# Performance work log

Measured on AMD Instinct MI355X. Metric: run time of the kernel, lower is better.

## Reference

```python
import jax, jax.numpy as jnp
import numpy as np

EPS = 1e-6
T_MAX = 0.999  # occlusion threshold used by compute_paths


def _dot(a, b):
    return jnp.sum(a * b, axis=-1)


def _mirror(p, v, n):
    # Reflect point p across plane through v with unit normal n.
    return p - 2.0 * _dot(p - v, n)[..., None] * n


def image_method(frm, to, mirror_v, mirror_n):
    """frm/to: [...,3]; mirror_v/mirror_n: [...,order,3] -> paths [...,order,3]."""
    order = mirror_v.shape[-2]
    images = []
    cur = frm
    for i in range(order):  # forward pass: successive images of TX
        cur = _mirror(cur, mirror_v[..., i, :], mirror_n[..., i, :])
        images.append(cur)
    paths = [None] * order
    nxt = to
    for i in range(order - 1, -1, -1):  # backward pass: intersect with planes
        img = images[i]
        v = mirror_v[..., i, :]
        n = mirror_n[..., i, :]
        d = nxt - img
        denom = _dot(d, n)
        t = _dot(v - img, n) / jnp.where(jnp.abs(denom) < EPS, EPS, denom)
        nxt = img + t[..., None] * d
        paths[i] = nxt
    return jnp.stack(paths, axis=-2)


def triangles_contain(tv, p):
    """tv: [...,3,3] triangle vertices, p: [...,3] point in same plane -> bool."""
    v0, v1, v2 = tv[..., 0, :], tv[..., 1, :], tv[..., 2, :]
    n0 = jnp.cross(p - v0, v1 - v0)
    n1 = jnp.cross(p - v1, v2 - v1)
    n2 = jnp.cross(p - v2, v0 - v2)
    d01, d12, d20 = _dot(n0, n1), _dot(n1, n2), _dot(n2, n0)
    pos = (d01 >= 0) & (d12 >= 0) & (d20 >= 0)
    neg = (d01 <= 0) & (d12 <= 0) & (d20 <= 0)
    return pos | neg


def same_side_of_mirrors(full_paths, mirror_v, mirror_n):
    """full_paths: [...,order+2,3]; consecutive vertices around each mirror on same side."""
    order = mirror_v.shape[-2]
    prev_v = full_paths[..., :order, :]
    next_v = full_paths[..., 2:, :]
    d_prev = _dot(prev_v - mirror_v, mirror_n)
    d_next = _dot(next_v - mirror_v, mirror_n)
    return d_prev * d_next >= 0


def rays_intersect_triangles(o, d, tv):
    """Moller-Trumbore. o,d: [...,3]; tv: broadcastable [...,3,3] -> (t, hit)."""
    v0, v1, v2 = tv[..., 0, :], tv[..., 1, :], tv[..., 2, :]
    e1 = v1 - v0
    e2 = v2 - v0
    h = jnp.cross(d, e2)
    a = _dot(e1, h)
    inv = 1.0 / jnp.where(jnp.abs(a) < EPS, 1.0, a)
    s = o - v0
    u = _dot(s, h) * inv
    q = jnp.cross(s, e1)
    v = _dot(d, q) * inv
    t = _dot(e2, q) * inv
    hit = (jnp.abs(a) > EPS) & (u >= 0.0) & (v >= 0.0) & (u + v <= 1.0) & (t > EPS)
    return t, hit


def compute_paths(transmitters, receivers, vertices, normals, triangles, path_candidates):
    P = path_candidates.shape[0]
    ntx = transmitters.shape[0]
    nrx = receivers.shape[0]
    all_tv = vertices[triangles]  # [T,3,3]

    frm = jnp.broadcast_to(transmitters[None, :, None, :], (P, ntx, nrx, 3))
    to = jnp.broadcast_to(receivers[None, None, :, :], (P, ntx, nrx, 3))

    pc_tv = all_tv[path_candidates]          # [P,order,3,3]
    mirror_v = pc_tv[..., 0, :]              # [P,order,3]
    mirror_n = normals[path_candidates]      # [P,order,3]
    tvb = pc_tv[:, None, None]               # [P,1,1,order,3,3]
    mvb = mirror_v[:, None, None]            # [P,1,1,order,3]
    mnb = mirror_n[:, None, None]

    paths = image_method(frm, to, mvb, mnb)  # [P,ntx,nrx,order,3]
    mask = jnp.all(triangles_contain(tvb, paths), axis=-1)

    full_paths = jnp.concatenate(
        (frm[..., None, :], paths, to[..., None, :]), axis=-2
    )  # [P,ntx,nrx,order+2,3]
    mask = mask & jnp.all(same_side_of_mirrors(full_paths, mvb, mnb), axis=-1)

    # Occlusion test: each of the order+1 segments vs every mesh triangle.
    ray_o = full_paths[..., :-1, None, :]       # [P,ntx,nrx,order+1,1,3]
    ray_d = jnp.diff(full_paths, axis=-2)[..., None, :]
    t, hit = rays_intersect_triangles(ray_o, ray_d, all_tv)  # [P,ntx,nrx,order+1,T]
    intersect = jnp.any((t < T_MAX) & hit, axis=(-1, -2))
    mask = mask & ~intersect

    # jit-friendly masking (original uses boolean fancy-indexing): zero-out invalid paths.
    return jnp.where(mask[..., None, None], full_paths, 0.0)


def setup_inputs() -> dict:
    key = jax.random.key(0)
    k1, k2, k3, k4 = jax.random.split(key, 4)
    V, T = 100, 128
    transmitters = 5.0 * jax.random.normal(k1, (1, 3), jnp.float32)
    receivers = 5.0 * jax.random.normal(k2, (1, 3), jnp.float32)
    vertices = jax.random.uniform(k3, (V, 3), jnp.float32, -10.0, 10.0)
    triangles = jax.random.randint(k4, (T, 3), 0, V, jnp.int32)
    tv = vertices[triangles]
    n = jnp.cross(tv[:, 1] - tv[:, 0], tv[:, 2] - tv[:, 0])
    normals = n / (jnp.linalg.norm(n, axis=-1, keepdims=True) + 1e-8)
    # generate_all_path_candidates(T, order=2): all ordered pairs (i,j), i != j
    idx = np.arange(T)
    ii, jj = np.meshgrid(idx, idx, indexing="ij")
    m = ii != jj
    path_candidates = jnp.asarray(np.stack([ii[m], jj[m]], axis=-1), jnp.int32)
    return {
        "transmitters": transmitters,
        "receivers": receivers,
        "vertices": vertices,
        "normals": normals,
        "triangles": triangles,
        "path_candidates": path_candidates,
        "order": 2,
    }


def reference(transmitters, receivers, vertices, normals, triangles, path_candidates, order):
    del order  # encoded in path_candidates.shape[-1]
    return compute_paths(transmitters, receivers, vertices, normals, triangles, path_candidates)
```

## Files before the change

kernel.cpp:

```cpp
#include <hip/hip_runtime.h>
#include <hip/hip_bf16.h>

#define EPS_F  1e-6f
#define TMAX_F 0.999f

struct F3 { float x, y, z; };

__device__ __forceinline__ F3 operator-(F3 a, F3 b){ return {a.x-b.x, a.y-b.y, a.z-b.z}; }
__device__ __forceinline__ F3 operator+(F3 a, F3 b){ return {a.x+b.x, a.y+b.y, a.z+b.z}; }
__device__ __forceinline__ F3 operator*(float s, F3 a){ return {s*a.x, s*a.y, s*a.z}; }
__device__ __forceinline__ float dot3(F3 a, F3 b){ return a.x*b.x + a.y*b.y + a.z*b.z; }
__device__ __forceinline__ F3 cross3(F3 a, F3 b){
  return { a.y*b.z - a.z*b.y, a.z*b.x - a.x*b.z, a.x*b.y - a.y*b.x };
}
__device__ __forceinline__ F3 ld3(const float* p){ return {p[0], p[1], p[2]}; }

__device__ __forceinline__ F3 mirror3(F3 p, F3 v, F3 n){
  float d = dot3(p - v, n);
  return p - (2.0f * d) * n;
}

__device__ __forceinline__ F3 plane_pt(F3 img, F3 v, F3 n, F3 nxt){
  F3 d = nxt - img;
  float den = dot3(d, n);
  float sd = (fabsf(den) < EPS_F) ? EPS_F : den;
  float t = dot3(v - img, n) / sd;
  return img + t * d;
}

__device__ __forceinline__ bool tri_contains(const float* tv9, F3 p){
  F3 a = ld3(tv9), b = ld3(tv9+3), c = ld3(tv9+6);
  F3 n0 = cross3(p - a, b - a);
  F3 n1 = cross3(p - b, c - b);
  F3 n2 = cross3(p - c, a - c);
  float d01 = dot3(n0, n1), d12 = dot3(n1, n2), d20 = dot3(n2, n0);
  bool pos = (d01 >= 0.f) & (d12 >= 0.f) & (d20 >= 0.f);
  bool neg = (d01 <= 0.f) & (d12 <= 0.f) & (d20 <= 0.f);
  return pos | neg;
}

__device__ __forceinline__ bool mt_block(F3 o, F3 d, const float* tv9){
  F3 a = ld3(tv9), b = ld3(tv9+3), c = ld3(tv9+6);
  F3 e1 = b - a, e2 = c - a;
  F3 h = cross3(d, e2);
  float det = dot3(e1, h);
  float safep = (fabsf(det) < EPS_F) ? 1.0f : det;
  float inv = 1.0f / safep;
  F3 s = o - a;
  float u = dot3(s, h) * inv;
  F3 q = cross3(s, e1);
  float v = dot3(d, q) * inv;
  float t = dot3(e2, q) * inv;
  bool hit = (fabsf(det) > EPS_F) & (u >= 0.f) & (v >= 0.f) & (u + v <= 1.f) & (t > EPS_F);
  return hit & (t < TMAX_F);
}

__global__ void __launch_bounds__(64)
paths_kernel(const float* __restrict__ txs, const float* __restrict__ rxs,
             const float* __restrict__ vertices, const float* __restrict__ normals,
             const int* __restrict__ triangles, const int* __restrict__ pc,
             int ntx, int nrx, int P, int T, float* __restrict__ out)
{
  extern __shared__ float smem[];
  float* tvS = smem;
  float* nS  = tvS + T * 9;
  float* fpS = nS + T * 3;

  const int lane = threadIdx.x;
  for (int i = lane; i < T * 3; i += 64) {
    int vi = triangles[i];
    tvS[i*3+0] = vertices[vi*3+0];
    tvS[i*3+1] = vertices[vi*3+1];
    tvS[i*3+2] = vertices[vi*3+2];
    nS[i] = normals[i];
  }
  __syncthreads();

  const long long total = (long long)P * ntx * nrx;
  const long long c = (long long)blockIdx.x * 64 + lane;
  const bool valid = c < total;
  const long long cc = valid ? c : 0;

  const int txrx = ntx * nrx;
  const int p  = (int)(cc / txrx);
  const int r  = (int)(cc % txrx);
  const int tx = r / nrx;
  const int rx = r % nrx;

  const F3 frm = ld3(txs + tx * 3);
  const F3 to  = ld3(rxs + rx * 3);

  const int t0 = pc[p*2 + 0];
  const int t1 = pc[p*2 + 1];

  const F3 v0 = ld3(tvS + t0 * 9);
  const F3 n0 = ld3(nS + t0 * 3);
  const F3 v1 = ld3(tvS + t1 * 9);
  const F3 n1 = ld3(nS + t1 * 3);

  const F3 img0 = mirror3(frm,  v0, n0);
  const F3 img1 = mirror3(img0, v1, n1);
  const F3 p1 = plane_pt(img1, v1, n1, to);
  const F3 p0 = plane_pt(img0, v0, n0, p1);

  bool mask = tri_contains(tvS + t0 * 9, p0) & tri_contains(tvS + t1 * 9, p1);
  float sp0 = dot3(frm - v0, n0) * dot3(p1 - v0, n0);
  float sp1 = dot3(p0  - v1, n1) * dot3(to - v1, n1);
  mask = mask & (sp0 >= 0.f) & (sp1 >= 0.f) & valid;

  float* myfp = fpS + lane * 12;
  myfp[0]=frm.x; myfp[1]=frm.y; myfp[2]=frm.z;
  myfp[3]=p0.x;  myfp[4]=p0.y;  myfp[5]=p0.z;
  myfp[6]=p1.x;  myfp[7]=p1.y;  myfp[8]=p1.z;
  myfp[9]=to.x;  myfp[10]=to.y; myfp[11]=to.z;
  __syncthreads();

  unsigned long long alive = __ballot(mask);
  unsigned long long occl = 0ULL;
  while (alive) {
    const int s = __builtin_ctzll(alive);
    alive &= alive - 1;
    const float* sfp = fpS + s * 12;
    F3 fp[4] = { ld3(sfp), ld3(sfp+3), ld3(sfp+6), ld3(sfp+9) };
    bool inter = false;
    #pragma unroll
    for (int seg = 0; seg < 3; ++seg) {
      F3 o = fp[seg];
      F3 d = fp[seg+1] - fp[seg];
      for (int tri = lane; tri < T; tri += 64) {
        inter |= mt_block(o, d, tvS + tri * 9);
      }
      if (__ballot(inter)) break;
    }
    if (__ballot(inter)) occl |= (1ULL << s);
  }

  const bool final_mask = mask && !((occl >> lane) & 1ULL);

  if (valid) {
    float4* o4 = reinterpret_cast<float4*>(out + (size_t)c * 12);
    if (final_mask) {
      o4[0] = make_float4(frm.x, frm.y, frm.z, p0.x);
      o4[1] = make_float4(p0.y,  p0.z,  p1.x,  p1.y);
      o4[2] = make_float4(p1.z,  to.x,  to.y,  to.z);
    } else {
      float4 z = make_float4(0.f, 0.f, 0.f, 0.f);
      o4[0] = z; o4[1] = z; o4[2] = z;
    }
  }
}

extern "C" void kernel_launch(void* const* d_in, const int* in_sizes, int n_in,
                              void* d_out, int out_size, void* d_ws, size_t ws_size,
                              hipStream_t stream) {
  const float* txs       = (const float*)d_in[0];
  const float* rxs       = (const float*)d_in[1];
  const float* vertices  = (const float*)d_in[2];
  const float* normals   = (const float*)d_in[3];
  const int*   triangles = (const int*)d_in[4];
  const int*   pc        = (const int*)d_in[5];

  const int ntx = in_sizes[0] / 3;
  const int nrx = in_sizes[1] / 3;
  const int T   = in_sizes[4] / 3;
  const int P   = in_sizes[5] / 2;

  float* out = (float*)d_out;

  const long long total = (long long)P * ntx * nrx;
  const int grid = (int)((total + 63) / 64);
  const size_t shmem = (size_t)(T * 12 + 64 * 12) * sizeof(float);

  paths_kernel<<<grid, 64, shmem, stream>>>(
      txs, rxs, vertices, normals, triangles, pc, ntx, nrx, P, T, out);
}
```

Measured before the change: 75.20 us.

## Spread occlusion tests across four wavefronts per block and coalesce output stores

```diff
diff --git a/kernel.cpp b/kernel.cpp
--- a/kernel.cpp
+++ b/kernel.cpp
@@ -55,7 +55,7 @@
   return hit & (t < TMAX_F);
 }
 
-__global__ void __launch_bounds__(64)
+__global__ void __launch_bounds__(256)
 paths_kernel(const float* __restrict__ txs, const float* __restrict__ rxs,
              const float* __restrict__ vertices, const float* __restrict__ normals,
              const int* __restrict__ triangles, const int* __restrict__ pc,
@@ -65,87 +65,107 @@
   float* tvS = smem;
   float* nS  = tvS + T * 9;
   float* fpS = nS + T * 3;
+  unsigned int* maskS = reinterpret_cast<unsigned int*>(fpS + 64 * 12);
+  unsigned int* occlS = maskS + 2;
 
-  const int lane = threadIdx.x;
-  for (int i = lane; i < T * 3; i += 64) {
+  const int tid  = threadIdx.x;
+  const int lane = tid & 63;
+  const int wid  = tid >> 6;
+
+  for (int i = tid; i < T * 3; i += 256) {
     int vi = triangles[i];
     tvS[i*3+0] = vertices[vi*3+0];
     tvS[i*3+1] = vertices[vi*3+1];
     tvS[i*3+2] = vertices[vi*3+2];
     nS[i] = normals[i];
   }
+  if (tid < 64) occlS[tid] = 0u;
   __syncthreads();
 
   const long long total = (long long)P * ntx * nrx;
-  const long long c = (long long)blockIdx.x * 64 + lane;
-  const bool valid = c < total;
-  const long long cc = valid ? c : 0;
+  const long long cbase = (long long)blockIdx.x * 64;
 
-  const int txrx = ntx * nrx;
-  const int p  = (int)(cc / txrx);
-  const int r  = (int)(cc % txrx);
-  const int tx = r / nrx;
-  const int rx = r % nrx;
+  if (wid == 0) {
+    const long long c = cbase + lane;
+    const bool valid = c < total;
+    const long long cc = valid ? c : 0;
 
-  const F3 frm = ld3(txs + tx * 3);
-  const F3 to  = ld3(rxs + rx * 3);
+    const int txrx = ntx * nrx;
+    const int p  = (int)(cc / txrx);
+    const int r  = (int)(cc % txrx);
+    const int tx = r / nrx;
+    const int rx = r % nrx;
 
-  const int t0 = pc[p*2 + 0];
-  const int t1 = pc[p*2 + 1];
+    const F3 frm = ld3(txs + tx * 3);
+    const F3 to  = ld3(rxs + rx * 3);
 
-  const F3 v0 = ld3(tvS + t0 * 9);
-  const F3 n0 = ld3(nS + t0 * 3);
-  const F3 v1 = ld3(tvS + t1 * 9);
-  const F3 n1 = ld3(nS + t1 * 3);
+    const int t0 = pc[p*2 + 0];
+    const int t1 = pc[p*2 + 1];
 
-  const F3 img0 = mirror3(frm,  v0, n0);
-  const F3 img1 = mirror3(img0, v1, n1);
-  const F3 p1 = plane_pt(img1, v1, n1, to);
-  const F3 p0 = plane_pt(img0, v0, n0, p1);
+    const F3 v0 = ld3(tvS + t0 * 9);
+    const F3 n0 = ld3(nS + t0 * 3);
+    const F3 v1 = ld3(tvS + t1 * 9);
+    const F3 n1 = ld3(nS + t1 * 3);
 
-  bool mask = tri_contains(tvS + t0 * 9, p0) & tri_contains(tvS + t1 * 9, p1);
-  float sp0 = dot3(frm - v0, n0) * dot3(p1 - v0, n0);
-  float sp1 = dot3(p0  - v1, n1) * dot3(to - v1, n1);
-  mask = mask & (sp0 >= 0.f) & (sp1 >= 0.f) & valid;
+    const F3 img0 = mirror3(frm,  v0, n0);
+    const F3 img1 = mirror3(img0, v1, n1);
+    const F3 p1 = plane_pt(img1, v1, n1, to);
+    const F3 p0 = plane_pt(img0, v0, n0, p1);
 
-  float* myfp = fpS + lane * 12;
-  myfp[0]=frm.x; myfp[1]=frm.y; myfp[2]=frm.z;
-  myfp[3]=p0.x;  myfp[4]=p0.y;  myfp[5]=p0.z;
-  myfp[6]=p1.x;  myfp[7]=p1.y;  myfp[8]=p1.z;
-  myfp[9]=to.x;  myfp[10]=to.y; myfp[11]=to.z;
+    bool mask = tri_contains(tvS + t0 * 9, p0) & tri_contains(tvS + t1 * 9, p1);
+    float sp0 = dot3(frm - v0, n0) * dot3(p1 - v0, n0);
+    float sp1 = dot3(p0  - v1, n1) * dot3(to - v1, n1);
+    mask = mask & (sp0 >= 0.f) & (sp1 >= 0.f) & valid;
+
+    float* myfp = fpS + lane * 12;
+    myfp[0]=frm.x; myfp[1]=frm.y; myfp[2]=frm.z;
+    myfp[3]=p0.x;  myfp[4]=p0.y;  myfp[5]=p0.z;
+    myfp[6]=p1.x;  myfp[7]=p1.y;  myfp[8]=p1.z;
+    myfp[9]=to.x;  myfp[10]=to.y; myfp[11]=to.z;
+
+    unsigned long long m = __ballot(mask);
+    if (lane == 0) {
+      maskS[0] = (unsigned int)(m & 0xffffffffu);
+      maskS[1] = (unsigned int)(m >> 32);
+    }
+  }
   __syncthreads();
 
-  unsigned long long alive = __ballot(mask);
-  unsigned long long occl = 0ULL;
-  while (alive) {
-    const int s = __builtin_ctzll(alive);
-    alive &= alive - 1;
-    const float* sfp = fpS + s * 12;
-    F3 fp[4] = { ld3(sfp), ld3(sfp+3), ld3(sfp+6), ld3(sfp+9) };
-    bool inter = false;
-    #pragma unroll
-    for (int seg = 0; seg < 3; ++seg) {
-      F3 o = fp[seg];
-      F3 d = fp[seg+1] - fp[seg];
-      for (int tri = lane; tri < T; tri += 64) {
-        inter |= mt_block(o, d, tvS + tri * 9);
+  {
+    unsigned long long alive =
+        ((unsigned long long)maskS[1] << 32) | (unsigned long long)maskS[0];
+    int item = 0;
+    while (alive) {
+      const int s = __builtin_ctzll(alive);
+      alive &= alive - 1;
+      const float* sfp = fpS + s * 12;
+      #pragma unroll
+      for (int seg = 0; seg < 3; ++seg, ++item) {
+        if ((item & 3) != wid) continue;
+        F3 o = ld3(sfp + seg * 3);
+        F3 e = ld3(sfp + seg * 3 + 3);
+        F3 d = e - o;
+        bool inter = false;
+        for (int tri = lane; tri < T; tri += 64)
+          inter |= mt_block(o, d, tvS + tri * 9);
+        unsigned long long hb = __ballot(inter);
+        if (lane == 0 && hb) occlS[s] = 1u;
       }
-      if (__ballot(inter)) break;
     }
-    if (__ballot(inter)) occl |= (1ULL << s);
   }
+  __syncthreads();
 
-  const bool final_mask = mask && !((occl >> lane) & 1ULL);
-
-  if (valid) {
-    float4* o4 = reinterpret_cast<float4*>(out + (size_t)c * 12);
-    if (final_mask) {
-      o4[0] = make_float4(frm.x, frm.y, frm.z, p0.x);
-      o4[1] = make_float4(p0.y,  p0.z,  p1.x,  p1.y);
-      o4[2] = make_float4(p1.z,  to.x,  to.y,  to.z);
-    } else {
-      float4 z = make_float4(0.f, 0.f, 0.f, 0.f);
-      o4[0] = z; o4[1] = z; o4[2] = z;
+  if (tid < 192) {
+    const int cand = tid / 3;
+    const int quad = tid - cand * 3;
+    const long long c = cbase + cand;
+    if (c < total) {
+      const unsigned int mw = maskS[cand >> 5];
+      const bool fin = ((mw >> (cand & 31)) & 1u) && !occlS[cand];
+      const float* fp = fpS + cand * 12 + quad * 4;
+      float4 val = fin ? make_float4(fp[0], fp[1], fp[2], fp[3])
+                       : make_float4(0.f, 0.f, 0.f, 0.f);
+      reinterpret_cast<float4*>(out)[c * 3 + quad] = val;
     }
   }
 }
@@ -169,8 +189,8 @@
 
   const long long total = (long long)P * ntx * nrx;
   const int grid = (int)((total + 63) / 64);
-  const size_t shmem = (size_t)(T * 12 + 64 * 12) * sizeof(float);
+  const size_t shmem = (size_t)(T * 12 + 64 * 12 + 2 + 64) * sizeof(float);
 
-  paths_kernel<<<grid, 64, shmem, stream>>>(
+  paths_kernel<<<grid, 256, shmem, stream>>>(
       txs, rxs, vertices, normals, triangles, pc, ntx, nrx, P, T, out);
 }
```

Result: faster. 70.27 us (-6.6%).

## Drop shared-memory triangle staging; gather vertices from global and shuffle path points

Applied to the files above, without the earlier changes.

```diff
diff --git a/kernel.cpp b/kernel.cpp
--- a/kernel.cpp
+++ b/kernel.cpp
@@ -15,6 +15,14 @@
 }
 __device__ __forceinline__ F3 ld3(const float* p){ return {p[0], p[1], p[2]}; }
 
+__device__ __forceinline__ void ld_tri(const int* __restrict__ tri,
+                                       const float* __restrict__ vtx,
+                                       int t, F3& a, F3& b, F3& c){
+  a = ld3(vtx + tri[t*3+0]*3);
+  b = ld3(vtx + tri[t*3+1]*3);
+  c = ld3(vtx + tri[t*3+2]*3);
+}
+
 __device__ __forceinline__ F3 mirror3(F3 p, F3 v, F3 n){
   float d = dot3(p - v, n);
   return p - (2.0f * d) * n;
@@ -28,8 +36,7 @@
   return img + t * d;
 }
 
-__device__ __forceinline__ bool tri_contains(const float* tv9, F3 p){
-  F3 a = ld3(tv9), b = ld3(tv9+3), c = ld3(tv9+6);
+__device__ __forceinline__ bool tri_contains(F3 a, F3 b, F3 c, F3 p){
   F3 n0 = cross3(p - a, b - a);
   F3 n1 = cross3(p - b, c - b);
   F3 n2 = cross3(p - c, a - c);
@@ -39,8 +46,7 @@
   return pos | neg;
 }
 
-__device__ __forceinline__ bool mt_block(F3 o, F3 d, const float* tv9){
-  F3 a = ld3(tv9), b = ld3(tv9+3), c = ld3(tv9+6);
+__device__ __forceinline__ bool mt_block(F3 o, F3 d, F3 a, F3 b, F3 c){
   F3 e1 = b - a, e2 = c - a;
   F3 h = cross3(d, e2);
   float det = dot3(e1, h);
@@ -59,33 +65,22 @@
 paths_kernel(const float* __restrict__ txs, const float* __restrict__ rxs,
              const float* __restrict__ vertices, const float* __restrict__ normals,
              const int* __restrict__ triangles, const int* __restrict__ pc,
-             int ntx, int nrx, int P, int T, float* __restrict__ out)
+             int ntx, int nrx, int total, int T, float* __restrict__ out)
 {
-  extern __shared__ float smem[];
-  float* tvS = smem;
-  float* nS  = tvS + T * 9;
-  float* fpS = nS + T * 3;
-
   const int lane = threadIdx.x;
-  for (int i = lane; i < T * 3; i += 64) {
-    int vi = triangles[i];
-    tvS[i*3+0] = vertices[vi*3+0];
-    tvS[i*3+1] = vertices[vi*3+1];
-    tvS[i*3+2] = vertices[vi*3+2];
-    nS[i] = normals[i];
-  }
-  __syncthreads();
-
-  const long long total = (long long)P * ntx * nrx;
-  const long long c = (long long)blockIdx.x * 64 + lane;
+  const int c = blockIdx.x * 64 + lane;
   const bool valid = c < total;
-  const long long cc = valid ? c : 0;
+  const int cc = valid ? c : 0;
 
   const int txrx = ntx * nrx;
-  const int p  = (int)(cc / txrx);
-  const int r  = (int)(cc % txrx);
-  const int tx = r / nrx;
-  const int rx = r % nrx;
+  int p, tx, rx;
+  if (txrx == 1) { p = cc; tx = 0; rx = 0; }
+  else {
+    p = cc / txrx;
+    const int r = cc - p * txrx;
+    tx = r / nrx;
+    rx = r - tx * nrx;
+  }
 
   const F3 frm = ld3(txs + tx * 3);
   const F3 to  = ld3(rxs + rx * 3);
@@ -93,42 +88,43 @@
   const int t0 = pc[p*2 + 0];
   const int t1 = pc[p*2 + 1];
 
-  const F3 v0 = ld3(tvS + t0 * 9);
-  const F3 n0 = ld3(nS + t0 * 3);
-  const F3 v1 = ld3(tvS + t1 * 9);
-  const F3 n1 = ld3(nS + t1 * 3);
+  F3 a0, b0, c0, a1, b1, c1;
+  ld_tri(triangles, vertices, t0, a0, b0, c0);
+  ld_tri(triangles, vertices, t1, a1, b1, c1);
+  const F3 n0 = ld3(normals + t0 * 3);
+  const F3 n1 = ld3(normals + t1 * 3);
+  const F3 v0 = a0;
+  const F3 v1 = a1;
 
   const F3 img0 = mirror3(frm,  v0, n0);
   const F3 img1 = mirror3(img0, v1, n1);
   const F3 p1 = plane_pt(img1, v1, n1, to);
   const F3 p0 = plane_pt(img0, v0, n0, p1);
 
-  bool mask = tri_contains(tvS + t0 * 9, p0) & tri_contains(tvS + t1 * 9, p1);
+  bool mask = tri_contains(a0, b0, c0, p0) & tri_contains(a1, b1, c1, p1);
   float sp0 = dot3(frm - v0, n0) * dot3(p1 - v0, n0);
   float sp1 = dot3(p0  - v1, n1) * dot3(to - v1, n1);
   mask = mask & (sp0 >= 0.f) & (sp1 >= 0.f) & valid;
-
-  float* myfp = fpS + lane * 12;
-  myfp[0]=frm.x; myfp[1]=frm.y; myfp[2]=frm.z;
-  myfp[3]=p0.x;  myfp[4]=p0.y;  myfp[5]=p0.z;
-  myfp[6]=p1.x;  myfp[7]=p1.y;  myfp[8]=p1.z;
-  myfp[9]=to.x;  myfp[10]=to.y; myfp[11]=to.z;
-  __syncthreads();
 
   unsigned long long alive = __ballot(mask);
   unsigned long long occl = 0ULL;
   while (alive) {
     const int s = __builtin_ctzll(alive);
     alive &= alive - 1;
-    const float* sfp = fpS + s * 12;
-    F3 fp[4] = { ld3(sfp), ld3(sfp+3), ld3(sfp+6), ld3(sfp+9) };
+    F3 fp[4];
+    fp[0] = { __shfl(frm.x, s), __shfl(frm.y, s), __shfl(frm.z, s) };
+    fp[1] = { __shfl(p0.x,  s), __shfl(p0.y,  s), __shfl(p0.z,  s) };
+    fp[2] = { __shfl(p1.x,  s), __shfl(p1.y,  s), __shfl(p1.z,  s) };
+    fp[3] = { __shfl(to.x,  s), __shfl(to.y,  s), __shfl(to.z,  s) };
     bool inter = false;
     #pragma unroll
     for (int seg = 0; seg < 3; ++seg) {
       F3 o = fp[seg];
       F3 d = fp[seg+1] - fp[seg];
-      for (int tri = lane; tri < T; tri += 64) {
-        inter |= mt_block(o, d, tvS + tri * 9);
+      for (int t = lane; t < T; t += 64) {
+        F3 ta, tb, tc;
+        ld_tri(triangles, vertices, t, ta, tb, tc);
+        inter |= mt_block(o, d, ta, tb, tc);
       }
       if (__ballot(inter)) break;
     }
@@ -169,8 +165,7 @@
 
   const long long total = (long long)P * ntx * nrx;
   const int grid = (int)((total + 63) / 64);
-  const size_t shmem = (size_t)(T * 12 + 64 * 12) * sizeof(float);
 
-  paths_kernel<<<grid, 64, shmem, stream>>>(
-      txs, rxs, vertices, normals, triangles, pc, ntx, nrx, P, T, out);
+  paths_kernel<<<grid, 64, 0, stream>>>(
+      txs, rxs, vertices, normals, triangles, pc, ntx, nrx, (int)total, T, out);
 }
```

Measured after the change: 74.93 us. About the same (-0.4%).
